# Performance work log

Measured on AMD Instinct MI355X. Metric: run time of the kernel, lower is better.

Reference implementation:

```python
import jax, jax.numpy as jnp
import numpy as np

B, P, K = 32, 2048, 20   # events, points per event, kNN neighbors
EPS = 1e-5               # BatchNorm eps (eval mode, running stats)


def setup_inputs() -> dict:
    key = jax.random.key(0)
    ks = iter(jax.random.split(key, 64))
    inp = {}
    inp["x"] = jax.random.normal(next(ks), (B * P, 7), jnp.float32)
    inp["batch"] = jnp.repeat(jnp.arange(B, dtype=jnp.int32), P)

    def add_layer(tag, cin, cout):
        inp["w" + tag] = jax.random.normal(next(ks), (cin, cout), jnp.float32) / np.sqrt(cin)
        inp["b" + tag] = jax.random.normal(next(ks), (cout,), jnp.float32) * 0.01
        inp["g" + tag] = jax.random.uniform(next(ks), (cout,), jnp.float32, 0.5, 1.5)
        inp["e" + tag] = jax.random.normal(next(ks), (cout,), jnp.float32) * 0.1
        inp["m" + tag] = jax.random.normal(next(ks), (cout,), jnp.float32) * 0.1
        inp["v" + tag] = jax.random.uniform(next(ks), (cout,), jnp.float32, 0.5, 1.5)

    # conv1 MLP: [14, 64, 64, 64]
    add_layer("10", 14, 64)
    add_layer("11", 64, 64)
    add_layer("12", 64, 64)
    # conv2 MLP: [128, 128]
    add_layer("20", 128, 128)
    return inp


def _lin_relu_bn(h, W, b, g, be, rm, rv):
    # Linear -> ReLU -> BatchNorm1d (eval mode: running stats)
    h = jax.nn.relu(h @ W + b)
    return (h - rm) * (g / jnp.sqrt(rv + EPS)) + be


def _knn_idx(x):
    # x: [B, P, C] -> indices of K nearest neighbors (incl. self), [B, P, K]
    sq = jnp.sum(x * x, axis=-1)                                   # [B, P]
    d = sq[:, :, None] + sq[:, None, :] - 2.0 * jnp.einsum("bpc,bqc->bpq", x, x)
    _, idx = jax.lax.top_k(-d, K)
    return idx


def _edge_conv(x, mlp):
    # DynamicEdgeConv: kNN graph on current features, edge MLP([x_i, x_j - x_i]), max-aggr
    idx = _knn_idx(x)                                              # [B, P, K]
    xj = jax.vmap(lambda xb, ib: xb[ib])(x, idx)                   # [B, P, K, C]
    xi = jnp.broadcast_to(x[:, :, None, :], xj.shape)
    e = jnp.concatenate([xi, xj - xi], axis=-1)                    # [B, P, K, 2C]
    return jnp.max(mlp(e), axis=2)                                 # [B, P, Cout]


def reference(x, batch,
              w10, b10, g10, e10, m10, v10,
              w11, b11, g11, e11, m11, v11,
              w12, b12, g12, e12, m12, v12,
              w20, b20, g20, e20, m20, v20):
    xb = x.reshape(B, P, -1)                                       # fixed-size events

    def mlp1(e):
        h = _lin_relu_bn(e, w10, b10, g10, e10, m10, v10)
        h = _lin_relu_bn(h, w11, b11, g11, e11, m11, v11)
        return _lin_relu_bn(h, w12, b12, g12, e12, m12, v12)

    def mlp2(e):
        return _lin_relu_bn(e, w20, b20, g20, e20, m20, v20)

    x1 = _edge_conv(xb, mlp1)                                      # [B, P, 64]
    x2 = _edge_conv(x1, mlp2)                                      # [B, P, 128]
    out = jnp.concatenate([x1, x2], axis=-1).reshape(B * P, 192)
    return out, batch
```

## Files before the change

kernel.cpp:

```cpp
#include <hip/hip_runtime.h>

#define B_EV 32
#define P_PT 2048
#define K_NN 20
#define NPTS (B_EV*P_PT)
#define EPS_BN 1e-5f
#define RINF 3.0e38f

typedef _Float16 half8 __attribute__((ext_vector_type(8)));
typedef float f32x4 __attribute__((ext_vector_type(4)));

static constexpr int oWA10=0, oWB10=448, oB10=896, oT10=960,
  oT11=5184,
  oT12=9408,
  oWA20=9472, oWB20=17664, oB20=25856, oT20=25984,
  oB11p=26048, oB12p=26112,
  oW11hi=26176, oW11lo=28224,
  oW12hi=30272, oW12lo=32320;
static constexpr size_t oIDX = 36864;
static constexpr size_t oA1  = 1347584;
static constexpr size_t oB1  = oA1 + (size_t)NPTS*64;
static constexpr size_t oV2  = oB1 + (size_t)NPTS*64;
static constexpr size_t oX1  = oV2 + (size_t)NPTS*128;
static constexpr size_t oSQ  = oX1 + (size_t)NPTS*64;
static constexpr size_t oD   = oSQ + (size_t)NPTS;
static constexpr size_t oU2  = oA1;

__global__ __launch_bounds__(128) void k_prep(
  const float* w10,const float* b10,const float* g10,const float* e10,const float* m10,const float* v10,
  const float* w11,const float* b11,const float* g11,const float* e11,const float* m11,const float* v11,
  const float* w12,const float* b12,const float* g12,const float* e12,const float* m12,const float* v12,
  const float* w20,const float* b20,const float* g20,const float* e20,const float* m20,const float* v20,
  float* ws)
{
  __shared__ float t10s[64], t11s[64];
  int c = threadIdx.x;
  if (c < 64) {
    float s0 = g10[c]*rsqrtf(v10[c]+EPS_BN);
    ws[oB10+c]=b10[c]*s0;
    float t10 = e10[c]-m10[c]*s0; ws[oT10+c]=t10; t10s[c]=t10;
    for (int i=0;i<7;i++){
      ws[oWA10+i*64+c]=(w10[i*64+c]-w10[(7+i)*64+c])*s0;
      ws[oWB10+i*64+c]=w10[(7+i)*64+c]*s0;
    }
    float s1 = g11[c]*rsqrtf(v11[c]+EPS_BN);
    float t11 = e11[c]-m11[c]*s1; ws[oT11+c]=t11; t11s[c]=t11;
    float s2 = g12[c]*rsqrtf(v12[c]+EPS_BN);
    ws[oT12+c]=e12[c]-m12[c]*s2;
  }
  __syncthreads();
  if (c < 64) {
    float s1 = g11[c]*rsqrtf(v11[c]+EPS_BN);
    _Float16* W1hi = (_Float16*)(ws + oW11hi);
    _Float16* W1lo = (_Float16*)(ws + oW11lo);
    float acc = b11[c]*s1;
    for (int i=0;i<64;i++){
      float wv = w11[i*64+c]*s1;
      _Float16 h = (_Float16)wv;
      W1hi[c*64+i] = h;
      W1lo[c*64+i] = (_Float16)(wv - (float)h);
      acc = fmaf(t10s[i], wv, acc);
    }
    ws[oB11p+c]=acc;
    float s2 = g12[c]*rsqrtf(v12[c]+EPS_BN);
    _Float16* W2hi = (_Float16*)(ws + oW12hi);
    _Float16* W2lo = (_Float16*)(ws + oW12lo);
    float acc2 = b12[c]*s2;
    for (int i=0;i<64;i++){
      float wv = w12[i*64+c]*s2;
      _Float16 h = (_Float16)wv;
      W2hi[c*64+i] = h;
      W2lo[c*64+i] = (_Float16)(wv - (float)h);
      acc2 = fmaf(t11s[i], wv, acc2);
    }
    ws[oB12p+c]=acc2;
  }
  {
    float s = g20[c]*rsqrtf(v20[c]+EPS_BN);
    ws[oB20+c]=b20[c]*s; ws[oT20+c]=e20[c]-m20[c]*s;
    for (int i=0;i<64;i++){
      ws[oWA20+i*128+c]=(w20[i*128+c]-w20[(64+i)*128+c])*s;
      ws[oWB20+i*128+c]=w20[(64+i)*128+c]*s;
    }
  }
}

__device__ __forceinline__ void select20(float (&d)[32], int lane, int base, int g,
                                         int* __restrict__ idxout)
{
  float g4[4];
  #pragma unroll
  for (int k=0;k<4;k++){
    float m = d[8*k];
    #pragma unroll
    for (int j=1;j<8;j++) m = fminf(m, d[8*k+j]);
    g4[k]=m;
  }
  float T = 0.f;
  #pragma unroll 1
  for (int pass=0; pass<20; ++pass){
    float m = fminf(fminf(g4[0],g4[1]), fminf(g4[2],g4[3]));
    #pragma unroll
    for (int off=32; off>0; off>>=1) m = fminf(m, __shfl_xor(m, off, 64));
    if (pass==19){ T=m; break; }
    #pragma unroll
    for (int k=0;k<4;k++){
      if (g4[k]==m){
        #pragma unroll
        for (int j=0;j<8;j++) d[8*k+j] = (d[8*k+j]==m) ? RINF : d[8*k+j];
        float mm = d[8*k];
        #pragma unroll
        for (int j=1;j<8;j++) mm = fminf(mm, d[8*k+j]);
        g4[k]=mm;
      }
    }
  }
  int cnt=0;
  #pragma unroll
  for (int j=0;j<32;j++){
    bool take = (d[j]>=RINF) || (d[j]==T);
    unsigned long long mb = __ballot(take);
    if (take){
      int pos = cnt + (int)__popcll(mb & ((1ull<<lane)-1ull));
      if (pos < K_NN) idxout[(size_t)g*K_NN + pos] = base + j*64 + lane;
    }
    cnt += (int)__popcll(mb);
  }
  if (lane==0){
    for (int r=cnt; r<K_NN; ++r) idxout[(size_t)g*K_NN + r] = g;
  }
}

__global__ __launch_bounds__(512) void k_knn1(const float* __restrict__ x, int* __restrict__ idxout)
{
  __shared__ float xs[P_PT*7];
  int t = threadIdx.x;
  int e = (int)(blockIdx.x >> 8);
  const float4* src = (const float4*)(x + (size_t)e*P_PT*7);
  #pragma unroll
  for (int u=0;u<7;u++) ((float4*)xs)[u*512+t] = src[u*512+t];
  __syncthreads();
  int lane = t & 63;
  int g = blockIdx.x*8 + (t>>6);
  int pin = g & (P_PT-1);
  float xp[7];
  #pragma unroll
  for (int i=0;i<7;i++) xp[i]=xs[pin*7+i];
  float d[32];
  #pragma unroll
  for (int j=0;j<32;j++){
    const float* xq = xs + (j*64+lane)*7;
    float s=0.f;
    #pragma unroll
    for (int i=0;i<7;i++){ float df=xp[i]-xq[i]; s=fmaf(df,df,s); }
    d[j]=s;
  }
  select20(d, lane, e*P_PT, g, idxout);
}

__global__ __launch_bounds__(256) void k_ab1(const float* __restrict__ x, const float* __restrict__ W,
                                             float* __restrict__ A1, float* __restrict__ B1)
{
  int g = blockIdx.x*256+threadIdx.x;
  float xi[7];
  #pragma unroll
  for (int i=0;i<7;i++) xi[i]=x[(size_t)g*7+i];
  float a[64], b[64];
  #pragma unroll
  for (int c=0;c<64;c++){ a[c]=W[oB10+c]; b[c]=0.f; }
  #pragma unroll
  for (int i=0;i<7;i++){
    #pragma unroll
    for (int c=0;c<64;c++) a[c]=fmaf(xi[i], W[oWA10+i*64+c], a[c]);
    #pragma unroll
    for (int c=0;c<64;c++) b[c]=fmaf(xi[i], W[oWB10+i*64+c], b[c]);
  }
  #pragma unroll
  for (int c=0;c<64;c+=4){
    float4 oa; oa.x=a[c]; oa.y=a[c+1]; oa.z=a[c+2]; oa.w=a[c+3];
    *(float4*)(A1+(size_t)g*64+c)=oa;
    float4 ob; ob.x=b[c]; ob.y=b[c+1]; ob.z=b[c+2]; ob.w=b[c+3];
    *(float4*)(B1+(size_t)g*64+c)=ob;
  }
}

__global__ __launch_bounds__(256, 2) void k_ec1m(const int* __restrict__ idx, const float* __restrict__ ws,
    const float* __restrict__ A1, const float* __restrict__ B1,
    float* __restrict__ x1, float* __restrict__ sqv, float* __restrict__ out)
{
  __shared__ _Float16 h2hi[4][32*64];
  __shared__ _Float16 h2lo[4][32*64];
  int t = threadIdx.x, w = t>>6, lane = t&63;
  int i = blockIdx.x*4 + w;
  int lg = lane>>4, lr = lane&15;

  int j0 = idx[(size_t)i*K_NN + lr];
  int j1 = (lr < 4) ? idx[(size_t)i*K_NN + 16 + lr] : i;

  f32x4 acc[2][4];
  #pragma unroll
  for (int nt=0;nt<4;nt++){
    float bb = ws[oB11p + nt*16 + lr];
    f32x4 v = {bb,bb,bb,bb};
    acc[0][nt]=v; acc[1][nt]=v;
  }
  {
    const _Float16* W1hi = (const _Float16*)(ws + oW11hi);
    const _Float16* W1lo = (const _Float16*)(ws + oW11lo);
    half8 wh[4][2], wl[4][2];
    #pragma unroll
    for (int nt=0;nt<4;nt++){
      #pragma unroll
      for (int ks=0;ks<2;ks++){
        wh[nt][ks] = *(const half8*)(W1hi + (nt*16+lr)*64 + ks*32 + lg*8);
        wl[nt][ks] = *(const half8*)(W1lo + (nt*16+lr)*64 + ks*32 + lg*8);
      }
    }
    const float* Ap = A1 + (size_t)i*64;
    #pragma unroll
    for (int m=0;m<2;m++){
      const float* Bp = B1 + (size_t)(m ? j1 : j0)*64;
      #pragma unroll
      for (int ks=0;ks<2;ks++){
        int c0 = ks*32 + lg*8;
        float4 b0 = *(const float4*)(Bp+c0);
        float4 b1 = *(const float4*)(Bp+c0+4);
        float4 a0 = *(const float4*)(Ap+c0);
        float4 a1 = *(const float4*)(Ap+c0+4);
        float hv[8];
        hv[0]=fmaxf(a0.x+b0.x,0.f); hv[1]=fmaxf(a0.y+b0.y,0.f);
        hv[2]=fmaxf(a0.z+b0.z,0.f); hv[3]=fmaxf(a0.w+b0.w,0.f);
        hv[4]=fmaxf(a1.x+b1.x,0.f); hv[5]=fmaxf(a1.y+b1.y,0.f);
        hv[6]=fmaxf(a1.z+b1.z,0.f); hv[7]=fmaxf(a1.w+b1.w,0.f);
        half8 ah, al;
        #pragma unroll
        for (int q=0;q<8;q++){
          _Float16 h = (_Float16)hv[q];
          ah[q]=h; al[q]=(_Float16)(hv[q]-(float)h);
        }
        #pragma unroll
        for (int nt=0;nt<4;nt++){
          acc[m][nt] = __builtin_amdgcn_mfma_f32_16x16x32_f16(ah, wh[nt][ks], acc[m][nt], 0,0,0);
          acc[m][nt] = __builtin_amdgcn_mfma_f32_16x16x32_f16(al, wh[nt][ks], acc[m][nt], 0,0,0);
          acc[m][nt] = __builtin_amdgcn_mfma_f32_16x16x32_f16(ah, wl[nt][ks], acc[m][nt], 0,0,0);
        }
      }
    }
  }

  _Float16* hbh = h2hi[w];
  _Float16* hbl = h2lo[w];
  #pragma unroll
  for (int m=0;m<2;m++){
    #pragma unroll
    for (int nt=0;nt<4;nt++){
      #pragma unroll
      for (int r=0;r<4;r++){
        int row = m*16 + lg*4 + r;
        int col = nt*16 + lr;
        int baddr = (row*128 + col*2) ^ ((row&7)<<4);
        float v = fmaxf(acc[m][nt][r], 0.f);
        _Float16 vh = (_Float16)v;
        *(_Float16*)((char*)hbh + baddr) = vh;
        *(_Float16*)((char*)hbl + baddr) = (_Float16)(v-(float)vh);
      }
    }
  }

  f32x4 acc2[2][4];
  #pragma unroll
  for (int nt=0;nt<4;nt++){
    float bb = ws[oB12p + nt*16 + lr];
    f32x4 v = {bb,bb,bb,bb};
    acc2[0][nt]=v; acc2[1][nt]=v;
  }
  {
    const _Float16* W2hi = (const _Float16*)(ws + oW12hi);
    const _Float16* W2lo = (const _Float16*)(ws + oW12lo);
    half8 wh[4][2], wl[4][2];
    #pragma unroll
    for (int nt=0;nt<4;nt++){
      #pragma unroll
      for (int ks=0;ks<2;ks++){
        wh[nt][ks] = *(const half8*)(W2hi + (nt*16+lr)*64 + ks*32 + lg*8);
        wl[nt][ks] = *(const half8*)(W2lo + (nt*16+lr)*64 + ks*32 + lg*8);
      }
    }
    #pragma unroll
    for (int m=0;m<2;m++){
      #pragma unroll
      for (int ks=0;ks<2;ks++){
        int row = m*16 + lr;
        int baddr = (row*128 + (ks*32 + lg*8)*2) ^ ((row&7)<<4);
        half8 ah = *(const half8*)((char*)hbh + baddr);
        half8 al = *(const half8*)((char*)hbl + baddr);
        #pragma unroll
        for (int nt=0;nt<4;nt++){
          acc2[m][nt] = __builtin_amdgcn_mfma_f32_16x16x32_f16(ah, wh[nt][ks], acc2[m][nt], 0,0,0);
          acc2[m][nt] = __builtin_amdgcn_mfma_f32_16x16x32_f16(al, wh[nt][ks], acc2[m][nt], 0,0,0);
          acc2[m][nt] = __builtin_amdgcn_mfma_f32_16x16x32_f16(ah, wl[nt][ks], acc2[m][nt], 0,0,0);
        }
      }
    }
  }

  float fin[4]; float sq = 0.f;
  #pragma unroll
  for (int nt=0;nt<4;nt++){
    float cv = -RINF;
    #pragma unroll
    for (int r=0;r<4;r++) cv = fmaxf(cv, acc2[0][nt][r]);
    if (lg==0){
      #pragma unroll
      for (int r=0;r<4;r++) cv = fmaxf(cv, acc2[1][nt][r]);
    }
    cv = fmaxf(cv, __shfl_xor(cv,16,64));
    cv = fmaxf(cv, __shfl_xor(cv,32,64));
    fin[nt] = fmaxf(cv, 0.f) + ws[oT12 + nt*16 + lr];
    sq = fmaf(fin[nt], fin[nt], sq);
  }
  if (lane < 16){
    #pragma unroll
    for (int nt=0;nt<4;nt++){
      x1[(size_t)i*64 + nt*16 + lane] = fin[nt];
      out[(size_t)i*192 + nt*16 + lane] = fin[nt];
    }
  }
  #pragma unroll
  for (int off=1; off<16; off<<=1) sq += __shfl_xor(sq, off, 64);
  if (lane == 0) sqv[i] = sq;
}

__global__ __launch_bounds__(256) void k_dist2(const float* __restrict__ x1, const float* __restrict__ sqv,
                                               float* __restrict__ D, int e0)
{
  __shared__ float As[64][68], Bs[64][68];
  int e = e0 + blockIdx.z;
  const float* Xe = x1 + (size_t)e*P_PT*64;
  int rb = blockIdx.y*64, cb = blockIdx.x*64;
  int t = threadIdx.x;
  int tr = t>>4, tk=(t&15)*4;
  #pragma unroll
  for (int rr=0;rr<4;rr++){
    int r = tr + 16*rr;
    float4 va = *(const float4*)(Xe + (size_t)(rb+r)*64 + tk);
    As[tk][r]=va.x; As[tk+1][r]=va.y; As[tk+2][r]=va.z; As[tk+3][r]=va.w;
    float4 vb = *(const float4*)(Xe + (size_t)(cb+r)*64 + tk);
    Bs[tk][r]=vb.x; Bs[tk+1][r]=vb.y; Bs[tk+2][r]=vb.z; Bs[tk+3][r]=vb.w;
  }
  __syncthreads();
  int tx=t&15, ty=t>>4;
  float acc[4][4];
  #pragma unroll
  for (int i=0;i<4;i++){
    #pragma unroll
    for (int j=0;j<4;j++) acc[i][j]=0.f;
  }
  #pragma unroll 4
  for (int k=0;k<64;k++){
    float4 a4 = *(const float4*)(&As[k][ty*4]);
    float4 b4 = *(const float4*)(&Bs[k][tx*4]);
    float a0=a4.x, a1=a4.y, a2=a4.z, a3=a4.w;
    float b0=b4.x, b1=b4.y, b2=b4.z, b3=b4.w;
    acc[0][0]=fmaf(a0,b0,acc[0][0]); acc[0][1]=fmaf(a0,b1,acc[0][1]);
    acc[0][2]=fmaf(a0,b2,acc[0][2]); acc[0][3]=fmaf(a0,b3,acc[0][3]);
    acc[1][0]=fmaf(a1,b0,acc[1][0]); acc[1][1]=fmaf(a1,b1,acc[1][1]);
    acc[1][2]=fmaf(a1,b2,acc[1][2]); acc[1][3]=fmaf(a1,b3,acc[1][3]);
    acc[2][0]=fmaf(a2,b0,acc[2][0]); acc[2][1]=fmaf(a2,b1,acc[2][1]);
    acc[2][2]=fmaf(a2,b2,acc[2][2]); acc[2][3]=fmaf(a2,b3,acc[2][3]);
    acc[3][0]=fmaf(a3,b0,acc[3][0]); acc[3][1]=fmaf(a3,b1,acc[3][1]);
    acc[3][2]=fmaf(a3,b2,acc[3][2]); acc[3][3]=fmaf(a3,b3,acc[3][3]);
  }
  float sr[4], sc[4];
  #pragma unroll
  for (int i=0;i<4;i++){ sr[i]=sqv[e*P_PT + rb+ty*4+i]; sc[i]=sqv[e*P_PT + cb+tx*4+i]; }
  #pragma unroll
  for (int i=0;i<4;i++){
    float4 o;
    o.x = sr[i]+sc[0]-2.f*acc[i][0];
    o.y = sr[i]+sc[1]-2.f*acc[i][1];
    o.z = sr[i]+sc[2]-2.f*acc[i][2];
    o.w = sr[i]+sc[3]-2.f*acc[i][3];
    *(float4*)(D + (size_t)(blockIdx.z*P_PT + rb+ty*4+i)*P_PT + cb + tx*4) = o;
  }
}

__global__ __launch_bounds__(256) void k_sel2(const float* __restrict__ D, int* __restrict__ idxout, int e0)
{
  int t=threadIdx.x, lane=t&63;
  int pl = blockIdx.x*4 + (t>>6);
  int le = pl>>11, pin = pl&(P_PT-1);
  int e = e0 + le;
  int g = e*P_PT + pin;
  const float* Dr = D + (size_t)pl*P_PT;
  float d[32];
  #pragma unroll
  for (int j=0;j<32;j++) d[j]=Dr[j*64+lane];
  select20(d, lane, e*P_PT, g, idxout);
}

__global__ __launch_bounds__(256) void k_uv2(const float* __restrict__ x1, const float* __restrict__ W,
                                             float* __restrict__ U2, float* __restrict__ V2)
{
  int g = blockIdx.x*256 + threadIdx.x;
  int half = blockIdx.y & 1;
  bool isU = blockIdx.y < 2;
  const float* Wb = W + (isU?oWA20:oWB20) + half*64;
  float acc[64];
  #pragma unroll
  for (int c=0;c<64;c++) acc[c] = isU ? W[oB20+half*64+c] : 0.f;
  const float* xp = x1 + (size_t)g*64;
  #pragma unroll 1
  for (int i=0;i<64;i+=4){
    float4 xv = *(const float4*)(xp+i);
    #pragma unroll
    for (int c=0;c<64;c++) acc[c]=fmaf(xv.x, Wb[(i+0)*128+c], acc[c]);
    #pragma unroll
    for (int c=0;c<64;c++) acc[c]=fmaf(xv.y, Wb[(i+1)*128+c], acc[c]);
    #pragma unroll
    for (int c=0;c<64;c++) acc[c]=fmaf(xv.z, Wb[(i+2)*128+c], acc[c]);
    #pragma unroll
    for (int c=0;c<64;c++) acc[c]=fmaf(xv.w, Wb[(i+3)*128+c], acc[c]);
  }
  float* dst = (isU?U2:V2) + (size_t)g*128 + half*64;
  #pragma unroll
  for (int c=0;c<64;c+=4){
    float4 o; o.x=acc[c]; o.y=acc[c+1]; o.z=acc[c+2]; o.w=acc[c+3];
    *(float4*)(dst+c)=o;
  }
}

__global__ __launch_bounds__(256) void k_gather2(const int* __restrict__ idx, const float* __restrict__ U2,
     const float* __restrict__ V2, const float* __restrict__ W, float* __restrict__ out)
{
  int g = blockIdx.x*256 + threadIdx.x;
  int half = blockIdx.y;
  float mx[64];
  #pragma unroll
  for (int c=0;c<64;c++) mx[c]=-RINF;
  for (int k=0;k<K_NN;k++){
    int j = idx[(size_t)g*K_NN+k];
    const float4* vp = (const float4*)(V2 + (size_t)j*128 + half*64);
    #pragma unroll
    for (int c4=0;c4<16;c4++){
      float4 v=vp[c4];
      mx[c4*4+0]=fmaxf(mx[c4*4+0],v.x);
      mx[c4*4+1]=fmaxf(mx[c4*4+1],v.y);
      mx[c4*4+2]=fmaxf(mx[c4*4+2],v.z);
      mx[c4*4+3]=fmaxf(mx[c4*4+3],v.w);
    }
  }
  const float* Up = U2 + (size_t)g*128 + half*64;
  float* op = out + (size_t)g*192 + 64 + half*64;
  #pragma unroll
  for (int c=0;c<64;c+=4){
    float4 o;
    o.x = fmaxf(Up[c+0]+mx[c+0],0.f)+W[oT20+half*64+c+0];
    o.y = fmaxf(Up[c+1]+mx[c+1],0.f)+W[oT20+half*64+c+1];
    o.z = fmaxf(Up[c+2]+mx[c+2],0.f)+W[oT20+half*64+c+2];
    o.w = fmaxf(Up[c+3]+mx[c+3],0.f)+W[oT20+half*64+c+3];
    *(float4*)(op+c)=o;
  }
}

__global__ __launch_bounds__(256) void k_batchf(const int* __restrict__ batch, float* __restrict__ out){
  int i = blockIdx.x*256+threadIdx.x;
  out[(size_t)NPTS*192 + i] = (float)batch[i];
}

extern "C" void kernel_launch(void* const* d_in, const int* in_sizes, int n_in,
                              void* d_out, int out_size, void* d_ws, size_t ws_size,
                              hipStream_t stream)
{
  const float* x     = (const float*)d_in[0];
  const int*   batch = (const int*)d_in[1];
  const float* w10=(const float*)d_in[2],  *b10=(const float*)d_in[3],  *g10=(const float*)d_in[4],
             *e10=(const float*)d_in[5],  *m10=(const float*)d_in[6],  *v10=(const float*)d_in[7];
  const float* w11=(const float*)d_in[8],  *b11=(const float*)d_in[9],  *g11=(const float*)d_in[10],
             *e11=(const float*)d_in[11], *m11=(const float*)d_in[12], *v11=(const float*)d_in[13];
  const float* w12=(const float*)d_in[14], *b12=(const float*)d_in[15], *g12=(const float*)d_in[16],
             *e12=(const float*)d_in[17], *m12=(const float*)d_in[18], *v12=(const float*)d_in[19];
  const float* w20=(const float*)d_in[20], *b20=(const float*)d_in[21], *g20=(const float*)d_in[22],
             *e20=(const float*)d_in[23], *m20=(const float*)d_in[24], *v20=(const float*)d_in[25];

  float* ws  = (float*)d_ws;
  float* out = (float*)d_out;
  int*   idxp = (int*)(ws + oIDX);

  k_prep<<<1,128,0,stream>>>(w10,b10,g10,e10,m10,v10, w11,b11,g11,e11,m11,v11,
                             w12,b12,g12,e12,m12,v12, w20,b20,g20,e20,m20,v20, ws);
  k_knn1<<<NPTS/8, 512, 0, stream>>>(x, idxp);
  k_ab1<<<NPTS/256, 256, 0, stream>>>(x, ws, ws+oA1, ws+oB1);
  k_ec1m<<<NPTS/4, 256, 0, stream>>>(idxp, ws, ws+oA1, ws+oB1, ws+oX1, ws+oSQ, out);

  size_t wsFloats = ws_size/4;
  long avail = (long)wsFloats - (long)oD;
  int CE = (int)(avail / (2048L*2048L));
  if (CE < 1) CE = 1;
  if (CE > 8) CE = 8;
  for (int e0=0; e0<B_EV; e0+=CE){
    int ce = (B_EV - e0 < CE) ? (B_EV - e0) : CE;
    k_dist2<<<dim3(32,32,ce),256,0,stream>>>(ws+oX1, ws+oSQ, ws+oD, e0);
    k_sel2<<<ce*512,256,0,stream>>>(ws+oD, idxp, e0);
  }

  k_uv2<<<dim3(NPTS/256,4),256,0,stream>>>(ws+oX1, ws, ws+oU2, ws+oV2);
  k_gather2<<<dim3(NPTS/256,2),256,0,stream>>>(idxp, ws+oU2, ws+oV2, ws, out);
  k_batchf<<<NPTS/256,256,0,stream>>>(batch, out);
}
```

Before: 1.182 ms.

## Remap block indices so each event stays on one XCD; reorder MFMA loops

Block IDs in knn1, ec1m, dist2 and gather2 are remapped so that blocks handling the same event land on the same XCD, given round-robin dispatch of consecutive block IDs across 8 XCDs. This is meant to improve L2 locality for the per-event data that gets gathered or reused (B1 neighbor rows, V2 rows, x1 tiles). In ec1m, the A/B loads and the hi/lo split are also hoisted ahead of the MFMA loop, and weights are loaded per output tile instead of all at once, which reduces register pressure. The mapping depends on the undocumented dispatch order, and the ce!=8 path uses a division.

```diff
diff --git a/kernel.cpp b/kernel.cpp
--- a/kernel.cpp
+++ b/kernel.cpp
@@ -135,13 +135,16 @@
 {
   __shared__ float xs[P_PT*7];
   int t = threadIdx.x;
-  int e = (int)(blockIdx.x >> 8);
+  int b = blockIdx.x;
+  int xcd = b & 7, kk = b >> 3;
+  int e = xcd + ((kk >> 8) << 3);
+  int blk = kk & 255;
   const float4* src = (const float4*)(x + (size_t)e*P_PT*7);
   #pragma unroll
   for (int u=0;u<7;u++) ((float4*)xs)[u*512+t] = src[u*512+t];
   __syncthreads();
   int lane = t & 63;
-  int g = blockIdx.x*8 + (t>>6);
+  int g = e*P_PT + blk*8 + (t>>6);
   int pin = g & (P_PT-1);
   float xp[7];
   #pragma unroll
@@ -191,11 +194,53 @@
   __shared__ _Float16 h2hi[4][32*64];
   __shared__ _Float16 h2lo[4][32*64];
   int t = threadIdx.x, w = t>>6, lane = t&63;
-  int i = blockIdx.x*4 + w;
+  int b = blockIdx.x;
+  int xcd = b & 7, kk = b >> 3;
+  int ev = xcd + ((kk >> 9) << 3);
+  int i = ev*P_PT + (kk & 511)*4 + w;
   int lg = lane>>4, lr = lane&15;
 
   int j0 = idx[(size_t)i*K_NN + lr];
   int j1 = (lr < 4) ? idx[(size_t)i*K_NN + 16 + lr] : i;
+
+  const float* Ap  = A1 + (size_t)i*64;
+  const float* Bp0 = B1 + (size_t)j0*64;
+  const float* Bp1 = B1 + (size_t)j1*64;
+  float4 av[2][2], bv[2][2][2];
+  #pragma unroll
+  for (int ks=0;ks<2;ks++){
+    int c0 = ks*32 + lg*8;
+    av[ks][0]    = *(const float4*)(Ap +c0);
+    av[ks][1]    = *(const float4*)(Ap +c0+4);
+    bv[0][ks][0] = *(const float4*)(Bp0+c0);
+    bv[0][ks][1] = *(const float4*)(Bp0+c0+4);
+    bv[1][ks][0] = *(const float4*)(Bp1+c0);
+    bv[1][ks][1] = *(const float4*)(Bp1+c0+4);
+  }
+
+  half8 AH[2][2], AL[2][2];
+  #pragma unroll
+  for (int m=0;m<2;m++){
+    #pragma unroll
+    for (int ks=0;ks<2;ks++){
+      float hv[8];
+      hv[0]=fmaxf(av[ks][0].x+bv[m][ks][0].x,0.f);
+      hv[1]=fmaxf(av[ks][0].y+bv[m][ks][0].y,0.f);
+      hv[2]=fmaxf(av[ks][0].z+bv[m][ks][0].z,0.f);
+      hv[3]=fmaxf(av[ks][0].w+bv[m][ks][0].w,0.f);
+      hv[4]=fmaxf(av[ks][1].x+bv[m][ks][1].x,0.f);
+      hv[5]=fmaxf(av[ks][1].y+bv[m][ks][1].y,0.f);
+      hv[6]=fmaxf(av[ks][1].z+bv[m][ks][1].z,0.f);
+      hv[7]=fmaxf(av[ks][1].w+bv[m][ks][1].w,0.f);
+      half8 ah, al;
+      #pragma unroll
+      for (int q=0;q<8;q++){
+        _Float16 h = (_Float16)hv[q];
+        ah[q]=h; al[q]=(_Float16)(hv[q]-(float)h);
+      }
+      AH[m][ks]=ah; AL[m][ks]=al;
+    }
+  }
 
   f32x4 acc[2][4];
   #pragma unroll
@@ -207,43 +252,22 @@
   {
     const _Float16* W1hi = (const _Float16*)(ws + oW11hi);
     const _Float16* W1lo = (const _Float16*)(ws + oW11lo);
-    half8 wh[4][2], wl[4][2];
     #pragma unroll
     for (int nt=0;nt<4;nt++){
+      const _Float16* whp = W1hi + (nt*16+lr)*64 + lg*8;
+      const _Float16* wlp = W1lo + (nt*16+lr)*64 + lg*8;
+      half8 wh0 = *(const half8*)(whp);
+      half8 wh1 = *(const half8*)(whp+32);
+      half8 wl0 = *(const half8*)(wlp);
+      half8 wl1 = *(const half8*)(wlp+32);
       #pragma unroll
-      for (int ks=0;ks<2;ks++){
-        wh[nt][ks] = *(const half8*)(W1hi + (nt*16+lr)*64 + ks*32 + lg*8);
-        wl[nt][ks] = *(const half8*)(W1lo + (nt*16+lr)*64 + ks*32 + lg*8);
-      }
-    }
-    const float* Ap = A1 + (size_t)i*64;
-    #pragma unroll
-    for (int m=0;m<2;m++){
-      const float* Bp = B1 + (size_t)(m ? j1 : j0)*64;
-      #pragma unroll
-      for (int ks=0;ks<2;ks++){
-        int c0 = ks*32 + lg*8;
-        float4 b0 = *(const float4*)(Bp+c0);
-        float4 b1 = *(const float4*)(Bp+c0+4);
-        float4 a0 = *(const float4*)(Ap+c0);
-        float4 a1 = *(const float4*)(Ap+c0+4);
-        float hv[8];
-        hv[0]=fmaxf(a0.x+b0.x,0.f); hv[1]=fmaxf(a0.y+b0.y,0.f);
-        hv[2]=fmaxf(a0.z+b0.z,0.f); hv[3]=fmaxf(a0.w+b0.w,0.f);
-        hv[4]=fmaxf(a1.x+b1.x,0.f); hv[5]=fmaxf(a1.y+b1.y,0.f);
-        hv[6]=fmaxf(a1.z+b1.z,0.f); hv[7]=fmaxf(a1.w+b1.w,0.f);
-        half8 ah, al;
-        #pragma unroll
-        for (int q=0;q<8;q++){
-          _Float16 h = (_Float16)hv[q];
-          ah[q]=h; al[q]=(_Float16)(hv[q]-(float)h);
-        }
-        #pragma unroll
-        for (int nt=0;nt<4;nt++){
-          acc[m][nt] = __builtin_amdgcn_mfma_f32_16x16x32_f16(ah, wh[nt][ks], acc[m][nt], 0,0,0);
-          acc[m][nt] = __builtin_amdgcn_mfma_f32_16x16x32_f16(al, wh[nt][ks], acc[m][nt], 0,0,0);
-          acc[m][nt] = __builtin_amdgcn_mfma_f32_16x16x32_f16(ah, wl[nt][ks], acc[m][nt], 0,0,0);
-        }
+      for (int m=0;m<2;m++){
+        acc[m][nt] = __builtin_amdgcn_mfma_f32_16x16x32_f16(AH[m][0], wh0, acc[m][nt], 0,0,0);
+        acc[m][nt] = __builtin_amdgcn_mfma_f32_16x16x32_f16(AL[m][0], wh0, acc[m][nt], 0,0,0);
+        acc[m][nt] = __builtin_amdgcn_mfma_f32_16x16x32_f16(AH[m][0], wl0, acc[m][nt], 0,0,0);
+        acc[m][nt] = __builtin_amdgcn_mfma_f32_16x16x32_f16(AH[m][1], wh1, acc[m][nt], 0,0,0);
+        acc[m][nt] = __builtin_amdgcn_mfma_f32_16x16x32_f16(AL[m][1], wh1, acc[m][nt], 0,0,0);
+        acc[m][nt] = __builtin_amdgcn_mfma_f32_16x16x32_f16(AH[m][1], wl1, acc[m][nt], 0,0,0);
       }
     }
   }
@@ -267,6 +291,18 @@
     }
   }
 
+  half8 AH2[2][2], AL2[2][2];
+  #pragma unroll
+  for (int m=0;m<2;m++){
+    #pragma unroll
+    for (int ks=0;ks<2;ks++){
+      int row = m*16 + lr;
+      int baddr = (row*128 + (ks*32 + lg*8)*2) ^ ((row&7)<<4);
+      AH2[m][ks] = *(const half8*)((char*)hbh + baddr);
+      AL2[m][ks] = *(const half8*)((char*)hbl + baddr);
+    }
+  }
+
   f32x4 acc2[2][4];
   #pragma unroll
   for (int nt=0;nt<4;nt++){
@@ -277,29 +313,22 @@
   {
     const _Float16* W2hi = (const _Float16*)(ws + oW12hi);
     const _Float16* W2lo = (const _Float16*)(ws + oW12lo);
-    half8 wh[4][2], wl[4][2];
     #pragma unroll
     for (int nt=0;nt<4;nt++){
+      const _Float16* whp = W2hi + (nt*16+lr)*64 + lg*8;
+      const _Float16* wlp = W2lo + (nt*16+lr)*64 + lg*8;
+      half8 wh0 = *(const half8*)(whp);
+      half8 wh1 = *(const half8*)(whp+32);
+      half8 wl0 = *(const half8*)(wlp);
+      half8 wl1 = *(const half8*)(wlp+32);
       #pragma unroll
-      for (int ks=0;ks<2;ks++){
-        wh[nt][ks] = *(const half8*)(W2hi + (nt*16+lr)*64 + ks*32 + lg*8);
-        wl[nt][ks] = *(const half8*)(W2lo + (nt*16+lr)*64 + ks*32 + lg*8);
-      }
-    }
-    #pragma unroll
-    for (int m=0;m<2;m++){
-      #pragma unroll
-      for (int ks=0;ks<2;ks++){
-        int row = m*16 + lr;
-        int baddr = (row*128 + (ks*32 + lg*8)*2) ^ ((row&7)<<4);
-        half8 ah = *(const half8*)((char*)hbh + baddr);
-        half8 al = *(const half8*)((char*)hbl + baddr);
-        #pragma unroll
-        for (int nt=0;nt<4;nt++){
-          acc2[m][nt] = __builtin_amdgcn_mfma_f32_16x16x32_f16(ah, wh[nt][ks], acc2[m][nt], 0,0,0);
-          acc2[m][nt] = __builtin_amdgcn_mfma_f32_16x16x32_f16(al, wh[nt][ks], acc2[m][nt], 0,0,0);
-          acc2[m][nt] = __builtin_amdgcn_mfma_f32_16x16x32_f16(ah, wl[nt][ks], acc2[m][nt], 0,0,0);
-        }
+      for (int m=0;m<2;m++){
+        acc2[m][nt] = __builtin_amdgcn_mfma_f32_16x16x32_f16(AH2[m][0], wh0, acc2[m][nt], 0,0,0);
+        acc2[m][nt] = __builtin_amdgcn_mfma_f32_16x16x32_f16(AL2[m][0], wh0, acc2[m][nt], 0,0,0);
+        acc2[m][nt] = __builtin_amdgcn_mfma_f32_16x16x32_f16(AH2[m][0], wl0, acc2[m][nt], 0,0,0);
+        acc2[m][nt] = __builtin_amdgcn_mfma_f32_16x16x32_f16(AH2[m][1], wh1, acc2[m][nt], 0,0,0);
+        acc2[m][nt] = __builtin_amdgcn_mfma_f32_16x16x32_f16(AL2[m][1], wh1, acc2[m][nt], 0,0,0);
+        acc2[m][nt] = __builtin_amdgcn_mfma_f32_16x16x32_f16(AH2[m][1], wl1, acc2[m][nt], 0,0,0);
       }
     }
   }
@@ -332,12 +361,17 @@
 }
 
 __global__ __launch_bounds__(256) void k_dist2(const float* __restrict__ x1, const float* __restrict__ sqv,
-                                               float* __restrict__ D, int e0)
+                                               float* __restrict__ D, int e0, int ce)
 {
   __shared__ float As[64][68], Bs[64][68];
-  int e = e0 + blockIdx.z;
+  int b = blockIdx.x;
+  int z, inner;
+  if (ce == 8){ z = b & 7; inner = b >> 3; }
+  else        { z = b / 1024; inner = b % 1024; }
+  int by = inner >> 5, bx = inner & 31;
+  int e = e0 + z;
   const float* Xe = x1 + (size_t)e*P_PT*64;
-  int rb = blockIdx.y*64, cb = blockIdx.x*64;
+  int rb = by*64, cb = bx*64;
   int t = threadIdx.x;
   int tr = t>>4, tk=(t&15)*4;
   #pragma unroll
@@ -381,7 +415,7 @@
     o.y = sr[i]+sc[1]-2.f*acc[i][1];
     o.z = sr[i]+sc[2]-2.f*acc[i][2];
     o.w = sr[i]+sc[3]-2.f*acc[i][3];
-    *(float4*)(D + (size_t)(blockIdx.z*P_PT + rb+ty*4+i)*P_PT + cb + tx*4) = o;
+    *(float4*)(D + (size_t)(z*P_PT + rb+ty*4+i)*P_PT + cb + tx*4) = o;
   }
 }
 
@@ -433,7 +467,10 @@
 __global__ __launch_bounds__(256) void k_gather2(const int* __restrict__ idx, const float* __restrict__ U2,
      const float* __restrict__ V2, const float* __restrict__ W, float* __restrict__ out)
 {
-  int g = blockIdx.x*256 + threadIdx.x;
+  int b = blockIdx.x;
+  int xcd = b & 7, kk = b >> 3;
+  int ev = xcd + ((kk >> 3) << 3);
+  int g = ev*P_PT + (kk & 7)*256 + threadIdx.x;
   int half = blockIdx.y;
   float mx[64];
   #pragma unroll
@@ -500,7 +537,7 @@
   if (CE > 8) CE = 8;
   for (int e0=0; e0<B_EV; e0+=CE){
     int ce = (B_EV - e0 < CE) ? (B_EV - e0) : CE;
-    k_dist2<<<dim3(32,32,ce),256,0,stream>>>(ws+oX1, ws+oSQ, ws+oD, e0);
+    k_dist2<<<ce*1024,256,0,stream>>>(ws+oX1, ws+oSQ, ws+oD, e0, ce);
     k_sel2<<<ce*512,256,0,stream>>>(ws+oD, idxp, e0);
   }
 
```

Result: no change. 1.171 ms (-0.9%).
